# Performance work log

Hardware: AMD Instinct MI355X
Metric: run time of the kernel (lower is better)

The kernel has to match this reference:

```python
import jax, jax.numpy as jnp
import numpy as np

N, H, W = 128, 128, 128
K = 9          # 3x3 kernel points
DIL = 3        # dilation of the deformable conv


def conv2d(x, w, pad, dil):
    # x: [N,C,H,W], w: [O,I,kh,kw]
    return jax.lax.conv_general_dilated(
        x, w, (1, 1), [(pad, pad), (pad, pad)], rhs_dilation=(dil, dil),
        dimension_numbers=("NCHW", "OIHW", "NCHW"))


def _bilinear_one(img, py, px):
    # img: [C,H,W]; py, px: [K,H,W] sample coords. Zero outside borders (DCNv2 semantics).
    Hh, Ww = img.shape[1], img.shape[2]
    y0f = jnp.floor(py)
    x0f = jnp.floor(px)
    y0 = y0f.astype(jnp.int32)
    x0 = x0f.astype(jnp.int32)
    ly = (py - y0f)[None]   # [1,K,H,W]
    lx = (px - x0f)[None]

    def gather(yi, xi):
        valid = ((yi >= 0) & (yi < Hh) & (xi >= 0) & (xi < Ww)).astype(img.dtype)
        yc = jnp.clip(yi, 0, Hh - 1)
        xc = jnp.clip(xi, 0, Ww - 1)
        return img[:, yc, xc] * valid[None]   # [C,K,H,W]

    v00 = gather(y0, x0)
    v01 = gather(y0, x0 + 1)
    v10 = gather(y0 + 1, x0)
    v11 = gather(y0 + 1, x0 + 1)
    return (v00 * (1 - ly) * (1 - lx) + v01 * (1 - ly) * lx
            + v10 * ly * (1 - lx) + v11 * ly * lx)


def modulated_deform_conv(x, offset, mod, w, b):
    # x: [N,C,H,W]; offset: [N,2K,H,W] with (dy,dx) interleaved per kernel point
    # (standard DCNv2 channel layout); mod: [N,K,H,W]; w: [O,C,3,3]; b: [O]
    Np, C, Hh, Ww = x.shape
    dy = offset[:, 0::2]   # [N,K,H,W]
    dx = offset[:, 1::2]
    base_y = ((jnp.repeat(jnp.arange(3), 3) - 1) * DIL).astype(x.dtype)  # [K]
    base_x = ((jnp.tile(jnp.arange(3), 3) - 1) * DIL).astype(x.dtype)
    gy = jnp.arange(Hh, dtype=x.dtype).reshape(1, 1, Hh, 1)
    gx = jnp.arange(Ww, dtype=x.dtype).reshape(1, 1, 1, Ww)
    py = dy + base_y.reshape(1, K, 1, 1) + gy   # [N,K,H,W]
    px = dx + base_x.reshape(1, K, 1, 1) + gx
    samp = jax.vmap(_bilinear_one)(x, py, px)   # [N,C,K,H,W]
    samp = samp * mod[:, None]                  # sigmoid modulation
    out = jnp.einsum("nckij,ock->noij", samp, w.reshape(w.shape[0], C, K))
    return out + b.reshape(1, -1, 1, 1)


def setup_inputs() -> dict:
    key = jax.random.key(0)
    ks = jax.random.split(key, 12)
    f32 = jnp.float32
    return {
        "mask": jax.random.normal(ks[0], (N, 1, H, W), f32),
        "x": jax.random.normal(ks[1], (N, 8, H, W), f32),
        "w1": jax.random.normal(ks[2], (2, 9, 3, 3), f32) * 0.1,      # conv1x1_1 (3x3)
        "b1": jnp.zeros((2,), f32),
        "w_off": jax.random.normal(ks[3], (27, 2, 3, 3), f32) * 0.05,  # offset/mask conv
        "w_dcn": jax.random.normal(ks[4], (2, 2, 3, 3), f32) * 0.2,    # deform conv weight
        "b_dcn": jnp.zeros((2,), f32),
        "w2": jax.random.normal(ks[5], (2, 2, 1, 1), f32) * 0.5,       # conv1x1_2
        "b2": jnp.zeros((2,), f32),
        "fc1_w": jax.random.normal(ks[6], (2048, 2 * 64 * 64), f32) * 0.01,
        "fc1_b": jnp.zeros((2048,), f32),
        "fc2_w": jax.random.normal(ks[7], (1024, 2048), f32) * 0.02,
        "fc2_b": jnp.zeros((1024,), f32),
        "io_w": jax.random.normal(ks[8], (1, 1024), f32) * 0.01,
        "io_b": jnp.zeros((1,), f32),
    }


def reference(mask, x, w1, b1, w_off, w_dcn, b_dcn, w2, b2,
              fc1_w, fc1_b, fc2_w, fc2_b, io_w, io_b):
    z = jnp.concatenate([x, mask], axis=1)                    # [N,9,H,W]
    h = conv2d(z, w1, 1, 1) + b1.reshape(1, -1, 1, 1)          # [N,2,H,W]
    om = conv2d(h, w_off, 3, 3)                               # [N,27,H,W], bias=False
    ox, oy, mm = jnp.split(om, 3, axis=1)
    offset = jnp.concatenate([ox, oy], axis=1)                # [N,18,H,W]
    mm = jax.nn.sigmoid(mm)                                   # [N,9,H,W]
    h = modulated_deform_conv(h, offset, mm, w_dcn, b_dcn)    # [N,2,H,W]
    h = jax.nn.relu(conv2d(h, w2, 0, 1) + b2.reshape(1, -1, 1, 1))
    Np, C, Hh, Ww = h.shape                                   # adaptive max pool to 64x64
    h = h.reshape(Np, C, 64, Hh // 64, 64, Ww // 64).max(axis=(3, 5))
    h = h.reshape(Np, -1)                                     # [N, 8192]
    h = jax.nn.relu(h @ fc1_w.T + fc1_b)
    h = jax.nn.relu(h @ fc2_w.T + fc2_b)
    return jax.nn.sigmoid(h @ io_w.T + io_b)                  # [N,1]
```

## Files before the change

### kernel.cpp

```cpp
#include <hip/hip_runtime.h>
#include <math.h>

#define NB   128
#define HH   128
#define WW   128
#define HW   (HH*WW)
#define POOLD 64
#define FC1_IN  8192
#define FC1_OUT 2048
#define FC2_OUT 1024

#define H1_OFF    0
#define POOL_OFF  4194304
#define FC1_OFF   5242880
#define FC2_OFF   5505024

__global__ __launch_bounds__(256) void conv1_kernel(
    const float* __restrict__ xin, const float* __restrict__ mask,
    const float* __restrict__ w1, const float* __restrict__ b1,
    float* __restrict__ h1,
    float* __restrict__ o1, const float* __restrict__ bb1,
    float* __restrict__ o2, const float* __restrict__ bb2)
{
    __shared__ float sw[164];
    __shared__ float sh[9][10][132];

    int tid = threadIdx.x;
    int n   = blockIdx.y;
    int r0  = blockIdx.x * 8;

    {
        int gi = (n * 16 + blockIdx.x) * 256 + tid;
        if (gi < NB * FC1_OUT) o1[gi] = bb1[gi & (FC1_OUT - 1)];
        if (gi < NB * FC2_OUT) o2[gi] = bb2[gi & (FC2_OUT - 1)];
    }

    if (tid < 162) sw[tid] = w1[tid];
    if (tid < 2)   sw[162 + tid] = b1[tid];

    for (int i = tid; i < 90; i += 256) {
        int c  = i / 10;
        int ry = i - c * 10;
        sh[c][ry][0]   = 0.f;
        sh[c][ry][129] = 0.f;
    }

    for (int idx = tid; idx < 2880; idx += 256) {
        int c   = idx / 320;
        int rem = idx - c * 320;
        int ry  = rem >> 5;
        int x4  = (rem & 31) << 2;
        int g   = r0 - 1 + ry;
        float4 v = make_float4(0.f, 0.f, 0.f, 0.f);
        if (g >= 0 && g < HH) {
            const float* src = (c < 8) ? (xin + ((size_t)n * 8 + c) * HW)
                                       : (mask + (size_t)n * HW);
            v = *(const float4*)(src + (size_t)g * WW + x4);
        }
        float* d = &sh[c][ry][x4 + 1];
        d[0] = v.x; d[1] = v.y; d[2] = v.z; d[3] = v.w;
    }
    __syncthreads();

    int x  = tid & 127;
    int yb = (tid >> 7) * 4;

    float acc[4][2];
    #pragma unroll
    for (int r = 0; r < 4; ++r) { acc[r][0] = sw[162]; acc[r][1] = sw[163]; }

    for (int c = 0; c < 9; ++c) {
        float v[6][3];
        #pragma unroll
        for (int iy = 0; iy < 6; ++iy)
            #pragma unroll
            for (int kx = 0; kx < 3; ++kx)
                v[iy][kx] = sh[c][yb + iy][x + kx];
        #pragma unroll
        for (int r = 0; r < 4; ++r)
            #pragma unroll
            for (int ky = 0; ky < 3; ++ky)
                #pragma unroll
                for (int kx = 0; kx < 3; ++kx) {
                    float t = v[r + ky][kx];
                    acc[r][0] += t * sw[c * 9 + ky * 3 + kx];
                    acc[r][1] += t * sw[81 + c * 9 + ky * 3 + kx];
                }
    }

    #pragma unroll
    for (int r = 0; r < 4; ++r) {
        size_t base = (size_t)n * (2 * HW) + (size_t)(r0 + yb + r) * WW + x;
        h1[base]      = acc[r][0];
        h1[base + HW] = acc[r][1];
    }
}

#define HALO_Y 5
#define HALO_X 6
#define SROWS  14
#define SCOLS  140

__device__ __forceinline__ void fetchg(
    const float* __restrict__ h0, const float* __restrict__ hb,
    int yi, int xi, float& a, float& b)
{
    a = 0.f; b = 0.f;
    if ((unsigned)yi < (unsigned)HH && (unsigned)xi < (unsigned)WW) {
        a = h0[yi * WW + xi];
        b = hb[yi * WW + xi];
    }
}

__global__ __launch_bounds__(256, 4) void fused_dcn_kernel(
    const float* __restrict__ h1,
    const float* __restrict__ w_off,
    const float* __restrict__ w_dcn,
    const float* __restrict__ b_dcn,
    const float* __restrict__ w2,
    const float* __restrict__ b2,
    float* __restrict__ pooled)
{
    __shared__ __align__(16) float sh[SROWS * SCOLS * 2];

    int tid = threadIdx.x;
    int n   = blockIdx.y;
    int r0  = blockIdx.x * 4;

    for (int i = tid; i < (SROWS * SCOLS * 2) / 4; i += 256)
        ((float4*)sh)[i] = make_float4(0.f, 0.f, 0.f, 0.f);
    __syncthreads();

    const float* h0g = h1 + (size_t)n * (2 * HW);
    const float* hbg = h0g + HW;

    for (int idx = tid; idx < SROWS * 32; idx += 256) {
        int ry = idx >> 5;
        int x4 = (idx & 31) << 2;
        int g  = r0 - HALO_Y + ry;
        if (g >= 0 && g < HH) {
            const float4 a = *(const float4*)(h0g + (size_t)g * WW + x4);
            const float4 b = *(const float4*)(hbg + (size_t)g * WW + x4);
            float* d = sh + (ry * SCOLS + HALO_X + x4) * 2;
            ((float4*)d)[0] = make_float4(a.x, b.x, a.y, b.y);
            ((float4*)d)[1] = make_float4(a.z, b.z, a.w, b.w);
        }
    }
    __syncthreads();

    int l  = tid & 63;
    int w  = tid >> 6;
    int xh = w & 1;
    int rp = w >> 1;
    int x  = l + 64 * xh;
    int yl0 = 2 * rp;
    int yg0 = r0 + yl0;

    int tb0 = ((yl0 + HALO_Y) * SCOLS + (x + HALO_X)) * 2;
    int tb1 = tb0 + SCOLS * 2;

    float h0a[9], h0b[9], h1a[9], h1b[9];
    #pragma unroll
    for (int t = 0; t < 9; ++t) {
        int off = ((t / 3 - 1) * 3 * SCOLS + (t % 3 - 1) * 3) * 2;
        h0a[t] = sh[tb0 + off]; h0b[t] = sh[tb0 + off + 1];
        h1a[t] = sh[tb1 + off]; h1b[t] = sh[tb1 + off + 1];
    }

    float a00 = 0.f, a01 = 0.f;
    float a10 = 0.f, a11 = 0.f;

    int lbase = (HALO_Y - r0) * SCOLS + HALO_X;

    #pragma unroll 1
    for (int k = 0; k < 9; ++k) {
        const float* wyp = w_off + (2 * k) * 18;
        const float* wxp = w_off + (2 * k + 1) * 18;
        const float* wmp = w_off + (18 + k) * 18;

        float dy0 = 0.f, dx0 = 0.f, mv0 = 0.f;
        float dy1 = 0.f, dx1 = 0.f, mv1 = 0.f;
        #pragma unroll
        for (int t = 0; t < 9; ++t) {
            float wyA = wyp[t], wyB = wyp[9 + t];
            float wxA = wxp[t], wxB = wxp[9 + t];
            float wmA = wmp[t], wmB = wmp[9 + t];
            dy0 += h0a[t] * wyA + h0b[t] * wyB;
            dx0 += h0a[t] * wxA + h0b[t] * wxB;
            mv0 += h0a[t] * wmA + h0b[t] * wmB;
            dy1 += h1a[t] * wyA + h1b[t] * wyB;
            dx1 += h1a[t] * wxA + h1b[t] * wxB;
            mv1 += h1a[t] * wmA + h1b[t] * wmB;
        }

        int bty = (k / 3 - 1) * 3, btx = (k % 3 - 1) * 3;
        float wd0 = w_dcn[k],      wd1 = w_dcn[9 + k];
        float wd2 = w_dcn[18 + k], wd3 = w_dcn[27 + k];

        {
            float mod = __builtin_amdgcn_rcpf(1.f + __expf(-mv0));
            float py  = (float)(yg0 + bty) + dy0;
            float px_ = (float)(x + btx) + dx0;
            float y0f = floorf(py), x0f = floorf(px_);
            int   y0 = (int)y0f,   x0i = (int)x0f;
            float ly = py - y0f,   lx = px_ - x0f;
            float A00, B00, A01, B01, A10, B10, A11, B11;
            if (fabsf(dy0) < 2.f && fabsf(dx0) < 3.f) {
                int p = (lbase + y0 * SCOLS + x0i) * 2;
                A00 = sh[p];             B00 = sh[p + 1];
                A01 = sh[p + 2];         B01 = sh[p + 3];
                A10 = sh[p + SCOLS * 2];     B10 = sh[p + SCOLS * 2 + 1];
                A11 = sh[p + SCOLS * 2 + 2]; B11 = sh[p + SCOLS * 2 + 3];
            } else {
                fetchg(h0g, hbg, y0,     x0i,     A00, B00);
                fetchg(h0g, hbg, y0,     x0i + 1, A01, B01);
                fetchg(h0g, hbg, y0 + 1, x0i,     A10, B10);
                fetchg(h0g, hbg, y0 + 1, x0i + 1, A11, B11);
            }
            float w00 = (1.f - ly) * (1.f - lx);
            float w01 = (1.f - ly) * lx;
            float w10 = ly * (1.f - lx);
            float w11 = ly * lx;
            float sA = (w00 * A00 + w01 * A01 + w10 * A10 + w11 * A11) * mod;
            float sB = (w00 * B00 + w01 * B01 + w10 * B10 + w11 * B11) * mod;
            a00 += wd0 * sA + wd1 * sB;
            a01 += wd2 * sA + wd3 * sB;
        }

        {
            float mod = __builtin_amdgcn_rcpf(1.f + __expf(-mv1));
            float py  = (float)(yg0 + 1 + bty) + dy1;
            float px_ = (float)(x + btx) + dx1;
            float y0f = floorf(py), x0f = floorf(px_);
            int   y0 = (int)y0f,   x0i = (int)x0f;
            float ly = py - y0f,   lx = px_ - x0f;
            float A00, B00, A01, B01, A10, B10, A11, B11;
            if (fabsf(dy1) < 2.f && fabsf(dx1) < 3.f) {
                int p = (lbase + y0 * SCOLS + x0i) * 2;
                A00 = sh[p];             B00 = sh[p + 1];
                A01 = sh[p + 2];         B01 = sh[p + 3];
                A10 = sh[p + SCOLS * 2];     B10 = sh[p + SCOLS * 2 + 1];
                A11 = sh[p + SCOLS * 2 + 2]; B11 = sh[p + SCOLS * 2 + 3];
            } else {
                fetchg(h0g, hbg, y0,     x0i,     A00, B00);
                fetchg(h0g, hbg, y0,     x0i + 1, A01, B01);
                fetchg(h0g, hbg, y0 + 1, x0i,     A10, B10);
                fetchg(h0g, hbg, y0 + 1, x0i + 1, A11, B11);
            }
            float w00 = (1.f - ly) * (1.f - lx);
            float w01 = (1.f - ly) * lx;
            float w10 = ly * (1.f - lx);
            float w11 = ly * lx;
            float sA = (w00 * A00 + w01 * A01 + w10 * A10 + w11 * A11) * mod;
            float sB = (w00 * B00 + w01 * B01 + w10 * B10 + w11 * B11) * mod;
            a10 += wd0 * sA + wd1 * sB;
            a11 += wd2 * sA + wd3 * sB;
        }
    }

    float bd0 = b_dcn[0], bd1 = b_dcn[1];
    float W20 = w2[0], W21 = w2[1], W22 = w2[2], W23 = w2[3];
    float B20 = b2[0], B21 = b2[1];

    float v00 = a00 + bd0, v01 = a01 + bd1;
    float u00 = fmaxf(W20 * v00 + W21 * v01 + B20, 0.f);
    float u01 = fmaxf(W22 * v00 + W23 * v01 + B21, 0.f);
    float v10 = a10 + bd0, v11 = a11 + bd1;
    float u10 = fmaxf(W20 * v10 + W21 * v11 + B20, 0.f);
    float u11 = fmaxf(W22 * v10 + W23 * v11 + B21, 0.f);
    float m0 = fmaxf(u00, u10);
    float m1 = fmaxf(u01, u11);

    m0 = fmaxf(m0, __shfl_xor(m0, 1, 64));
    m1 = fmaxf(m1, __shfl_xor(m1, 1, 64));

    if ((l & 1) == 0) {
        int pr = blockIdx.x * 2 + rp;
        int pc = (l >> 1) + 32 * xh;
        size_t pb = (size_t)n * FC1_IN + (size_t)pr * POOLD + pc;
        pooled[pb]        = m0;
        pooled[pb + 4096] = m1;
    }
}

typedef __bf16 bf16x8 __attribute__((ext_vector_type(8)));
typedef float  f32x4  __attribute__((ext_vector_type(4)));

#define LDT2 72

__device__ __forceinline__ unsigned short f2bf(float f) {
    unsigned int u = __float_as_uint(f);
    return (unsigned short)((u + 0x7fffu + ((u >> 16) & 1u)) >> 16);
}

__global__ __launch_bounds__(256, 4) void gemm_bf16_splitk(
    const float* __restrict__ A, const float* __restrict__ B,
    float* __restrict__ C, int K, int Nc, int kchunk, int relu_a)
{
    __shared__ __align__(16) unsigned short As[128 * LDT2];
    __shared__ __align__(16) unsigned short Bs[64 * LDT2];

    int tid = threadIdx.x;
    int jt  = blockIdx.x;
    int k0  = blockIdx.y * kchunk;
    int iters = kchunk >> 6;

    int t16 = tid >> 4;
    int c64 = (tid & 15) << 2;
    int t4  = tid >> 2;
    int cB  = (tid & 3) << 4;

    const float* Ag = A + (size_t)t16 * K + k0 + c64;
    const float* Bg = B + (size_t)(jt * 64 + t4) * K + k0 + cB;

    float4 pa[8]; float4 pb[4];
    #pragma unroll
    for (int p = 0; p < 8; ++p) pa[p] = *(const float4*)(Ag + (size_t)(p * 16) * K);
    #pragma unroll
    for (int q = 0; q < 4; ++q) pb[q] = *(const float4*)(Bg + q * 4);

    int lane = tid & 63;
    int w    = tid >> 6;
    int quad = lane >> 4;
    int r    = lane & 15;

    f32x4 acc[2][4];
    #pragma unroll
    for (int mt = 0; mt < 2; ++mt)
        #pragma unroll
        for (int nt = 0; nt < 4; ++nt)
            acc[mt][nt] = (f32x4){0.f, 0.f, 0.f, 0.f};

    for (int it = 0; it < iters; ++it) {
        #pragma unroll
        for (int p = 0; p < 8; ++p) {
            float4 v = pa[p];
            if (relu_a) {
                v.x = fmaxf(v.x, 0.f); v.y = fmaxf(v.y, 0.f);
                v.z = fmaxf(v.z, 0.f); v.w = fmaxf(v.w, 0.f);
            }
            ushort4 s = make_ushort4(f2bf(v.x), f2bf(v.y), f2bf(v.z), f2bf(v.w));
            *(ushort4*)&As[(t16 + p * 16) * LDT2 + c64] = s;
        }
        #pragma unroll
        for (int q = 0; q < 4; ++q) {
            float4 v = pb[q];
            ushort4 s = make_ushort4(f2bf(v.x), f2bf(v.y), f2bf(v.z), f2bf(v.w));
            *(ushort4*)&Bs[t4 * LDT2 + cB + q * 4] = s;
        }
        __syncthreads();

        if (it + 1 < iters) {
            Ag += 64; Bg += 64;
            #pragma unroll
            for (int p = 0; p < 8; ++p) pa[p] = *(const float4*)(Ag + (size_t)(p * 16) * K);
            #pragma unroll
            for (int q = 0; q < 4; ++q) pb[q] = *(const float4*)(Bg + q * 4);
        }

        #pragma unroll
        for (int ks = 0; ks < 2; ++ks) {
            bf16x8 af[2];
            #pragma unroll
            for (int mt = 0; mt < 2; ++mt)
                af[mt] = *(const bf16x8*)&As[(w * 32 + mt * 16 + r) * LDT2
                                             + ks * 32 + quad * 8];
            bf16x8 bfr[4];
            #pragma unroll
            for (int nt = 0; nt < 4; ++nt)
                bfr[nt] = *(const bf16x8*)&Bs[(nt * 16 + r) * LDT2
                                              + ks * 32 + quad * 8];

            #pragma unroll
            for (int mt = 0; mt < 2; ++mt)
                #pragma unroll
                for (int nt = 0; nt < 4; ++nt)
                    acc[mt][nt] = __builtin_amdgcn_mfma_f32_16x16x32_bf16(
                        af[mt], bfr[nt], acc[mt][nt], 0, 0, 0);
        }

        __syncthreads();
    }

    #pragma unroll
    for (int mt = 0; mt < 2; ++mt) {
        int mrow = w * 32 + mt * 16 + quad * 4;
        #pragma unroll
        for (int nt = 0; nt < 4; ++nt) {
            int col = jt * 64 + nt * 16 + r;
            #pragma unroll
            for (int i = 0; i < 4; ++i)
                atomicAdd(C + (size_t)(mrow + i) * Nc + col, acc[mt][nt][i]);
        }
    }
}

__global__ __launch_bounds__(256) void io_kernel(
    const float* __restrict__ fc2o, const float* __restrict__ io_w,
    const float* __restrict__ io_b, float* __restrict__ out)
{
    int n = blockIdx.x;
    int tid = threadIdx.x;
    float4 v = *(const float4*)(fc2o + (size_t)n * FC2_OUT + tid * 4);
    float4 wv = *(const float4*)(io_w + tid * 4);
    float s = fmaxf(v.x, 0.f) * wv.x + fmaxf(v.y, 0.f) * wv.y
            + fmaxf(v.z, 0.f) * wv.z + fmaxf(v.w, 0.f) * wv.w;
    #pragma unroll
    for (int off = 32; off > 0; off >>= 1)
        s += __shfl_down(s, off, 64);
    __shared__ float red[4];
    if ((tid & 63) == 0) red[tid >> 6] = s;
    __syncthreads();
    if (tid == 0) {
        float t = red[0] + red[1] + red[2] + red[3] + io_b[0];
        out[n] = 1.f / (1.f + expf(-t));
    }
}

extern "C" void kernel_launch(void* const* d_in, const int* in_sizes, int n_in,
                              void* d_out, int out_size, void* d_ws, size_t ws_size,
                              hipStream_t stream)
{
    const float* mask  = (const float*)d_in[0];
    const float* x     = (const float*)d_in[1];
    const float* w1    = (const float*)d_in[2];
    const float* b1    = (const float*)d_in[3];
    const float* w_off = (const float*)d_in[4];
    const float* w_dcn = (const float*)d_in[5];
    const float* b_dcn = (const float*)d_in[6];
    const float* w2    = (const float*)d_in[7];
    const float* b2    = (const float*)d_in[8];
    const float* fc1_w = (const float*)d_in[9];
    const float* fc1_b = (const float*)d_in[10];
    const float* fc2_w = (const float*)d_in[11];
    const float* fc2_b = (const float*)d_in[12];
    const float* io_w  = (const float*)d_in[13];
    const float* io_b  = (const float*)d_in[14];

    float* ws      = (float*)d_ws;
    float* h1      = ws + H1_OFF;
    float* pooled  = ws + POOL_OFF;
    float* fc1_out = ws + FC1_OFF;
    float* fc2_out = ws + FC2_OFF;
    float* out     = (float*)d_out;

    conv1_kernel<<<dim3(16, NB), 256, 0, stream>>>(
        x, mask, w1, b1, h1, fc1_out, fc1_b, fc2_out, fc2_b);

    fused_dcn_kernel<<<dim3(32, NB), 256, 0, stream>>>(
        h1, w_off, w_dcn, b_dcn, w2, b2, pooled);

    gemm_bf16_splitk<<<dim3(FC1_OUT / 64, 16), 256, 0, stream>>>(
        pooled, fc1_w, fc1_out, FC1_IN, FC1_OUT, FC1_IN / 16, 0);

    gemm_bf16_splitk<<<dim3(FC2_OUT / 64, 16), 256, 0, stream>>>(
        fc1_out, fc2_w, fc2_out, FC1_OUT, FC2_OUT, FC1_OUT / 16, 1);

    io_kernel<<<NB, 256, 0, stream>>>(fc2_out, io_w, io_b, out);
}
```

Baseline: 290.2 us.

## Replace split-K atomics with partial buffers and separate reductions

The split-K GEMMs now write per-split partial tiles to workspace instead of doing float atomicAdd into pre-initialised outputs. A new reduce kernel sums the FC1 partials and adds the bias, and the io kernel sums the FC2 partials plus bias itself. FC1 split count drops from 16 to 8. The bias initialisation is removed from conv1. The intent is to avoid atomic contention and make the results deterministic. In exchange it adds an extra launch and extra partial-buffer traffic, and the partials reuse the h1 workspace region, which is dead by then.

New measurement: 288.2 us. Within noise of the previous version (-0.7%).

```diff
diff --git a/kernel.cpp b/kernel.cpp
--- a/kernel.cpp
+++ b/kernel.cpp
@@ -10,6 +10,9 @@
 #define FC1_OUT 2048
 #define FC2_OUT 1024
 
+#define KS1  8
+#define KS2  16
+
 #define H1_OFF    0
 #define POOL_OFF  4194304
 #define FC1_OFF   5242880
@@ -18,9 +21,7 @@
 __global__ __launch_bounds__(256) void conv1_kernel(
     const float* __restrict__ xin, const float* __restrict__ mask,
     const float* __restrict__ w1, const float* __restrict__ b1,
-    float* __restrict__ h1,
-    float* __restrict__ o1, const float* __restrict__ bb1,
-    float* __restrict__ o2, const float* __restrict__ bb2)
+    float* __restrict__ h1)
 {
     __shared__ float sw[164];
     __shared__ float sh[9][10][132];
@@ -28,12 +29,6 @@
     int tid = threadIdx.x;
     int n   = blockIdx.y;
     int r0  = blockIdx.x * 8;
-
-    {
-        int gi = (n * 16 + blockIdx.x) * 256 + tid;
-        if (gi < NB * FC1_OUT) o1[gi] = bb1[gi & (FC1_OUT - 1)];
-        if (gi < NB * FC2_OUT) o2[gi] = bb2[gi & (FC2_OUT - 1)];
-    }
 
     if (tid < 162) sw[tid] = w1[tid];
     if (tid < 2)   sw[162 + tid] = b1[tid];
@@ -295,7 +290,7 @@
 
 __global__ __launch_bounds__(256, 4) void gemm_bf16_splitk(
     const float* __restrict__ A, const float* __restrict__ B,
-    float* __restrict__ C, int K, int Nc, int kchunk, int relu_a)
+    float* __restrict__ Cpart, int K, int Nc, int kchunk, int relu_a)
 {
     __shared__ __align__(16) unsigned short As[128 * LDT2];
     __shared__ __align__(16) unsigned short Bs[64 * LDT2];
@@ -382,6 +377,7 @@
         __syncthreads();
     }
 
+    float* Cp = Cpart + (size_t)blockIdx.y * (128 * Nc);
     #pragma unroll
     for (int mt = 0; mt < 2; ++mt) {
         int mrow = w * 32 + mt * 16 + quad * 4;
@@ -390,18 +386,42 @@
             int col = jt * 64 + nt * 16 + r;
             #pragma unroll
             for (int i = 0; i < 4; ++i)
-                atomicAdd(C + (size_t)(mrow + i) * Nc + col, acc[mt][nt][i]);
-        }
-    }
+                Cp[(size_t)(mrow + i) * Nc + col] = acc[mt][nt][i];
+        }
+    }
+}
+
+__global__ __launch_bounds__(256) void reduce_fc1_kernel(
+    const float* __restrict__ part, const float* __restrict__ bias,
+    float* __restrict__ outp)
+{
+    int i = blockIdx.x * 256 + threadIdx.x;
+    float4 s = ((const float4*)part)[i];
+    #pragma unroll
+    for (int p = 1; p < KS1; ++p) {
+        float4 v = ((const float4*)part)[(size_t)p * (NB * FC1_OUT / 4) + i];
+        s.x += v.x; s.y += v.y; s.z += v.z; s.w += v.w;
+    }
+    float4 b = ((const float4*)bias)[i & (FC1_OUT / 4 - 1)];
+    s.x += b.x; s.y += b.y; s.z += b.z; s.w += b.w;
+    ((float4*)outp)[i] = s;
 }
 
 __global__ __launch_bounds__(256) void io_kernel(
-    const float* __restrict__ fc2o, const float* __restrict__ io_w,
-    const float* __restrict__ io_b, float* __restrict__ out)
+    const float* __restrict__ part2, const float* __restrict__ fc2_b,
+    const float* __restrict__ io_w, const float* __restrict__ io_b,
+    float* __restrict__ out)
 {
     int n = blockIdx.x;
     int tid = threadIdx.x;
-    float4 v = *(const float4*)(fc2o + (size_t)n * FC2_OUT + tid * 4);
+    size_t base = (size_t)n * FC2_OUT + tid * 4;
+
+    float4 v = ((const float4*)fc2_b)[tid];
+    #pragma unroll
+    for (int p = 0; p < KS2; ++p) {
+        float4 t = *(const float4*)(part2 + (size_t)p * (NB * FC2_OUT) + base);
+        v.x += t.x; v.y += t.y; v.z += t.z; v.w += t.w;
+    }
     float4 wv = *(const float4*)(io_w + tid * 4);
     float s = fmaxf(v.x, 0.f) * wv.x + fmaxf(v.y, 0.f) * wv.y
             + fmaxf(v.z, 0.f) * wv.z + fmaxf(v.w, 0.f) * wv.w;
@@ -441,20 +461,23 @@
     float* h1      = ws + H1_OFF;
     float* pooled  = ws + POOL_OFF;
     float* fc1_out = ws + FC1_OFF;
-    float* fc2_out = ws + FC2_OFF;
+    float* part1   = ws + H1_OFF;
+    float* part2   = ws + H1_OFF + KS1 * (NB * FC1_OUT);
     float* out     = (float*)d_out;
 
-    conv1_kernel<<<dim3(16, NB), 256, 0, stream>>>(
-        x, mask, w1, b1, h1, fc1_out, fc1_b, fc2_out, fc2_b);
+    conv1_kernel<<<dim3(16, NB), 256, 0, stream>>>(x, mask, w1, b1, h1);
 
     fused_dcn_kernel<<<dim3(32, NB), 256, 0, stream>>>(
         h1, w_off, w_dcn, b_dcn, w2, b2, pooled);
 
-    gemm_bf16_splitk<<<dim3(FC1_OUT / 64, 16), 256, 0, stream>>>(
-        pooled, fc1_w, fc1_out, FC1_IN, FC1_OUT, FC1_IN / 16, 0);
-
-    gemm_bf16_splitk<<<dim3(FC2_OUT / 64, 16), 256, 0, stream>>>(
-        fc1_out, fc2_w, fc2_out, FC1_OUT, FC2_OUT, FC1_OUT / 16, 1);
-
-    io_kernel<<<NB, 256, 0, stream>>>(fc2_out, io_w, io_b, out);
-}
+    gemm_bf16_splitk<<<dim3(FC1_OUT / 64, KS1), 256, 0, stream>>>(
+        pooled, fc1_w, part1, FC1_IN, FC1_OUT, FC1_IN / KS1, 0);
+
+    reduce_fc1_kernel<<<NB * FC1_OUT / 4 / 256, 256, 0, stream>>>(
+        part1, fc1_b, fc1_out);
+
+    gemm_bf16_splitk<<<dim3(FC2_OUT / 64, KS2), 256, 0, stream>>>(
+        fc1_out, fc2_w, part2, FC1_OUT, FC2_OUT, FC1_OUT / KS2, 1);
+
+    io_kernel<<<NB, 256, 0, stream>>>(part2, fc2_b, io_w, io_b, out);
+}
```
